# Kernel optimization log

Measured on AMD Instinct MI355X. Metric: run time of the kernel, lower is better.

The kernel has to match this reference:

```python
import jax, jax.numpy as jnp
import numpy as np

EMBED_DIM = 512
NUM_HEADS = 8
TGT_LEN = 1024
BSZ = 16


def setup_inputs() -> dict:
    key = jax.random.key(0)
    ks = jax.random.split(key, 6)
    E = EMBED_DIM
    query = jax.random.normal(ks[0], (TGT_LEN, BSZ, E), jnp.float32)
    i_proj = jax.random.normal(ks[1], (3 * E,), jnp.float32)
    # xavier_uniform-ish scale for (3E, E)
    lim = (6.0 / (3 * E + E)) ** 0.5
    in_proj_weight = jax.random.uniform(ks[2], (3 * E, E), jnp.float32, -lim, lim)
    in_proj_bias = jnp.zeros((3 * E,), jnp.float32)
    lim2 = (6.0 / (2 * E)) ** 0.5
    out_w = jax.random.uniform(ks[3], (E, E), jnp.float32, -lim2, lim2)
    out_b = jnp.zeros((E,), jnp.float32)
    bias_k = jax.random.normal(ks[4], (1, 1, E), jnp.float32)
    bias_v = jax.random.normal(ks[5], (1, 1, E), jnp.float32)
    return dict(query=query, i_proj=i_proj, in_proj_weight=in_proj_weight,
                in_proj_bias=in_proj_bias, out_w=out_w, out_b=out_b,
                bias_k=bias_k, bias_v=bias_v)


def reference(query, i_proj, in_proj_weight, in_proj_bias, out_w, out_b, bias_k, bias_v):
    # qkv_same path: key = value = query (self-attention)
    T, B, E = query.shape
    H = NUM_HEADS
    hd = E // H
    scaling = hd ** -0.5
    # per-call weight mutation: every 3rd column replaced by i_proj
    w = in_proj_weight.at[:, ::3].set(i_proj[:, None])
    qkv = jnp.einsum('tbe,fe->tbf', query, w) + in_proj_bias  # (T, B, 3E)
    q, k, v = jnp.split(qkv, 3, axis=-1)
    q = q * scaling
    k = jnp.concatenate([k, jnp.broadcast_to(bias_k, (1, B, E))], axis=0)  # (T+1, B, E)
    v = jnp.concatenate([v, jnp.broadcast_to(bias_v, (1, B, E))], axis=0)
    S = k.shape[0]
    q = q.reshape(T, B * H, hd).transpose(1, 0, 2)  # (B*H, T, hd)
    k = k.reshape(S, B * H, hd).transpose(1, 0, 2)  # (B*H, S, hd)
    v = v.reshape(S, B * H, hd).transpose(1, 0, 2)
    aw = jnp.einsum('nth,nsh->nts', q, k)  # (B*H, T, S)
    # global min-max normalization over the entire score tensor (not softmax)
    mn = jnp.min(aw)
    mx = jnp.max(aw)
    aw = (aw - mn) / (mx - mn)
    attn = jnp.einsum('nts,nsh->nth', aw, v)  # (B*H, T, hd)
    attn = attn.transpose(1, 0, 2).reshape(T, B, E)
    attn = attn @ out_w.T + out_b  # out_proj
    aw_avg = aw.reshape(B, H, T, S).sum(axis=1) / H  # (B, T, S)
    wq, wk, wv = jnp.split(w, 3, axis=0)
    w_ret = jnp.stack([wq.T, wk.T, wv.T], axis=0)  # (3, E, E)
    return attn, aw_avg, w_ret
```

## Files before the change

kernel.cpp:

```cpp
#include <hip/hip_runtime.h>
#include <hip/hip_bf16.h>
#include <stdint.h>

typedef __bf16 bf16;
typedef __bf16 bf16x8 __attribute__((ext_vector_type(8)));
typedef __bf16 bf16x4 __attribute__((ext_vector_type(4)));
typedef float  f32x4  __attribute__((ext_vector_type(4)));

#define MFMA_BF16(a,b,c) __builtin_amdgcn_mfma_f32_16x16x32_bf16((a),(b),(c),0,0,0)

#define WS_QBF_IN  0L
#define WS_WBF     16777216L
#define WS_OUTWBF  18350080L
#define WS_Q       18874368L
#define WS_K       35651584L
#define WS_V       52428800L
#define WS_VT      69206016L
#define WS_AWLAST  85983232L
#define WS_VCS     86507520L
#define WS_MM      86540288L
#define WS_KT      86540544L
#define WS_KTV     103317760L

__device__ __forceinline__ void gload16(const void* g, void* l) {
  __builtin_amdgcn_global_load_lds((const __attribute__((address_space(1))) uint32_t*)g,
                                   (__attribute__((address_space(3))) uint32_t*)l, 16, 0, 0);
}
__device__ __forceinline__ unsigned ordf(float x) {
  unsigned b = __float_as_uint(x);
  return (b & 0x80000000u) ? ~b : (b | 0x80000000u);
}
__device__ __forceinline__ float deordf(unsigned u) {
  unsigned b = (u & 0x80000000u) ? (u ^ 0x80000000u) : ~u;
  return __uint_as_float(b);
}

__global__ __launch_bounds__(256) void prep_all_kernel(
    const float* __restrict__ query, bf16* __restrict__ qbf_out,
    const float* __restrict__ in_w, const float* __restrict__ i_proj,
    const float* __restrict__ out_w, bf16* __restrict__ w_bf,
    bf16* __restrict__ outw_bf, float* __restrict__ w_ret,
    unsigned* __restrict__ mm) {
  long idx = (long)blockIdx.x * 256 + threadIdx.x;
  if (idx == 0) { mm[0] = 0xFFFFFFFFu; mm[1] = 0u; }
  if (idx < 786432L) {
    int f = (int)(idx >> 9), e = (int)(idx & 511);
    float val = (e % 3 == 0) ? i_proj[f] : in_w[idx];
    w_bf[idx] = (bf16)val;
    w_ret[(long)(f >> 9) * 262144 + (long)e * 512 + (f & 511)] = val;
  } else if (idx < 1048576L) {
    long j = idx - 786432L;
    outw_bf[j] = (bf16)out_w[j];
  }
#pragma unroll
  for (int it = 0; it < 2; ++it) {
    long i = idx + (long)it * 1048576L;
    float4 v = ((const float4*)query)[i];
    bf16x4 o; o[0] = (bf16)v.x; o[1] = (bf16)v.y; o[2] = (bf16)v.z; o[3] = (bf16)v.w;
    ((bf16x4*)qbf_out)[i] = o;
  }
}

#define PIPE_STAGE(Abase_, Bbase_, kk_, buf_)                                      \
  do {                                                                             \
    _Pragma("unroll")                                                              \
    for (int i_ = 0; i_ < 4; ++i_) {                                               \
      int c_ = tid + i_ * 256;                                                     \
      int row_ = c_ >> 3;                                                          \
      int cc_ = (c_ & 7) ^ (row_ & 7);                                             \
      gload16((Abase_) + (long)row_ * 512 + (kk_) + cc_ * 8,                       \
              (char*)aT[buf_] + (i_ * 256 + w * 64) * 16);                         \
      gload16((Bbase_) + (long)row_ * 512 + (kk_) + cc_ * 8,                       \
              (char*)bT[buf_] + (i_ * 256 + w * 64) * 16);                         \
    }                                                                              \
  } while (0)

#define PIPE_COMPUTE(buf_)                                                         \
  do {                                                                             \
    _Pragma("unroll")                                                              \
    for (int ks_ = 0; ks_ < 2; ++ks_) {                                            \
      bf16x8 af[4], bfr[4];                                                        \
      _Pragma("unroll")                                                            \
      for (int mi_ = 0; mi_ < 4; ++mi_) {                                          \
        int r_ = rm + mi_ * 16 + l15;                                              \
        int p_ = (ks_ * 4 + l4) ^ (r_ & 7);                                        \
        af[mi_] = *(const bf16x8*)((const char*)aT[buf_] + r_ * 128 + p_ * 16);    \
      }                                                                            \
      _Pragma("unroll")                                                            \
      for (int ni_ = 0; ni_ < 4; ++ni_) {                                          \
        int r_ = cn + ni_ * 16 + l15;                                              \
        int p_ = (ks_ * 4 + l4) ^ (r_ & 7);                                        \
        bfr[ni_] = *(const bf16x8*)((const char*)bT[buf_] + r_ * 128 + p_ * 16);   \
      }                                                                            \
      _Pragma("unroll")                                                            \
      for (int mi_ = 0; mi_ < 4; ++mi_)                                            \
        _Pragma("unroll")                                                          \
        for (int ni_ = 0; ni_ < 4; ++ni_)                                          \
          acc[mi_][ni_] = MFMA_BF16(af[mi_], bfr[ni_], acc[mi_][ni_]);             \
    }                                                                              \
  } while (0)

template <int MODE, int MINW>
__global__ __launch_bounds__(256, MINW) void gemm_kernel(
    const bf16* __restrict__ A, const bf16* __restrict__ B,
    const float* __restrict__ bias,
    bf16* __restrict__ q_out, bf16* __restrict__ k_out, bf16* __restrict__ v_out,
    float* __restrict__ outC) {
  __shared__ __align__(16) bf16 aT[2][128 * 64];
  __shared__ __align__(16) bf16 bT[2][128 * 64];
  const int tid = threadIdx.x;
  const int lane = tid & 63, w = tid >> 6;
  const int l15 = lane & 15, l4 = lane >> 4;
  const long r0 = (long)blockIdx.y * 128;
  const long f0 = (long)blockIdx.x * 128;
  const int rm = (w >> 1) * 64, cn = (w & 1) * 64;
  const bf16* Ab = A + r0 * 512;
  const bf16* Bb = B + f0 * 512;
  f32x4 acc[4][4] = {};

  PIPE_STAGE(Ab, Bb, 0, 0);
  PIPE_STAGE(Ab, Bb, 64, 1);
  asm volatile("s_waitcnt vmcnt(8)" ::: "memory");
  __builtin_amdgcn_s_barrier();
  __builtin_amdgcn_sched_barrier(0);
#pragma unroll
  for (int k = 0; k < 8; ++k) {
    PIPE_COMPUTE(k & 1);
    __builtin_amdgcn_s_barrier();
    __builtin_amdgcn_sched_barrier(0);
    if (k + 2 < 8) PIPE_STAGE(Ab, Bb, (k + 2) * 64, k & 1);
    if (k + 1 < 8) {
      if (k + 2 < 8) asm volatile("s_waitcnt vmcnt(8)" ::: "memory");
      else           asm volatile("s_waitcnt vmcnt(0)" ::: "memory");
      __builtin_amdgcn_s_barrier();
      __builtin_amdgcn_sched_barrier(0);
    }
  }
#pragma unroll
  for (int mi = 0; mi < 4; ++mi)
#pragma unroll
    for (int ni = 0; ni < 4; ++ni)
#pragma unroll
      for (int r = 0; r < 4; ++r) {
        long row = r0 + rm + mi * 16 + l4 * 4 + r;
        int f = (int)f0 + cn + ni * 16 + l15;
        float val = acc[mi][ni][r] + bias[f];
        if (MODE == 0) {
          int t = (int)(row >> 4), b = (int)(row & 15);
          int which = f >> 9, hh = (f >> 6) & 7, d = f & 63;
          long off = ((long)(b * 8 + hh) * 1024 + t) * 64 + d;
          if (which == 0)      q_out[off] = (bf16)(val * 0.125f);
          else if (which == 1) k_out[off] = (bf16)val;
          else                 v_out[off] = (bf16)val;
        } else {
          outC[row * 512 + f] = val;
        }
      }
}

__global__ __launch_bounds__(256, 2) void awsum_gemm_kernel(
    const bf16* __restrict__ q_bf, const bf16* __restrict__ k_bf,
    bf16* __restrict__ aw_raw, unsigned* __restrict__ mm) {
  __shared__ __align__(16) char wlds[4][16384];
  const int tid = threadIdx.x;
  const int lane = tid & 63, w = tid >> 6;
  const int l15 = lane & 15, l4 = lane >> 4;
  const int bid = blockIdx.x;
  const int xcd = bid & 7, slot = bid >> 3;
  const int b = xcd * 2 + (slot >> 6);
  const int rest = slot & 63;
  const int t0 = (rest >> 2) * 64;
  const int s0w = (rest & 3) * 256 + w * 64;
  char* lA = wlds[w];
  char* lB = wlds[w] + 8192;

  f32x4 acc[4][4] = {};
  f32x4 snap[4][4] = {};
  float vmin = 1e30f, vmax = -1e30f;

#define WAVE_STAGE(k_, buf_)                                                          \
  do {                                                                                \
    const int hh_ = (k_) >> 1, kh_ = ((k_) & 1) * 32;                                 \
    const bf16* qb_ = q_bf + ((long)(b * 8 + hh_) * 1024 + t0) * 64 + kh_;            \
    const bf16* kb_ = k_bf + ((long)(b * 8 + hh_) * 1024 + s0w) * 64 + kh_;           \
    _Pragma("unroll")                                                                 \
    for (int i_ = 0; i_ < 4; ++i_) {                                                  \
      int ci_ = lane + i_ * 64;                                                       \
      int row_ = ci_ >> 2, cc_ = ci_ & 3;                                             \
      int cc2_ = cc_ ^ ((row_ >> 1) & 3);                                             \
      gload16(qb_ + (long)row_ * 64 + cc2_ * 8, lA + (buf_) * 4096 + i_ * 1024);      \
      gload16(kb_ + (long)row_ * 64 + cc2_ * 8, lB + (buf_) * 4096 + i_ * 1024);      \
    }                                                                                 \
  } while (0)

#define WAVE_COMPUTE(buf_)                                                            \
  do {                                                                                \
    bf16x8 af[4], bfr[4];                                                             \
    _Pragma("unroll")                                                                 \
    for (int mi_ = 0; mi_ < 4; ++mi_) {                                               \
      int r_ = mi_ * 16 + l15;                                                        \
      int p_ = l4 ^ ((r_ >> 1) & 3);                                                  \
      af[mi_] = *(const bf16x8*)(lA + (buf_) * 4096 + r_ * 64 + p_ * 16);             \
    }                                                                                 \
    _Pragma("unroll")                                                                 \
    for (int ni_ = 0; ni_ < 4; ++ni_) {                                               \
      int r_ = ni_ * 16 + l15;                                                        \
      int p_ = l4 ^ ((r_ >> 1) & 3);                                                  \
      bfr[ni_] = *(const bf16x8*)(lB + (buf_) * 4096 + r_ * 64 + p_ * 16);            \
    }                                                                                 \
    _Pragma("unroll")                                                                 \
    for (int mi_ = 0; mi_ < 4; ++mi_)                                                 \
      _Pragma("unroll")                                                               \
      for (int ni_ = 0; ni_ < 4; ++ni_)                                               \
        acc[mi_][ni_] = MFMA_BF16(af[mi_], bfr[ni_], acc[mi_][ni_]);                  \
  } while (0)

  WAVE_STAGE(0, 0);
  WAVE_STAGE(1, 1);
#pragma unroll
  for (int k = 0; k < 16; ++k) {
    if (k < 15) asm volatile("s_waitcnt vmcnt(8)" ::: "memory");
    else        asm volatile("s_waitcnt vmcnt(0)" ::: "memory");
    __builtin_amdgcn_sched_barrier(0);
    WAVE_COMPUTE(k & 1);
    if (k & 1) {
#pragma unroll
      for (int mi = 0; mi < 4; ++mi)
#pragma unroll
        for (int ni = 0; ni < 4; ++ni) {
          f32x4 d = acc[mi][ni] - snap[mi][ni];
#pragma unroll
          for (int r = 0; r < 4; ++r) {
            vmin = fminf(vmin, d[r]);
            vmax = fmaxf(vmax, d[r]);
          }
          snap[mi][ni] = acc[mi][ni];
        }
    }
    if (k + 2 < 16) {
      asm volatile("s_waitcnt lgkmcnt(0)" ::: "memory");
      __builtin_amdgcn_sched_barrier(0);
      WAVE_STAGE(k + 2, k & 1);
    }
  }
#pragma unroll
  for (int mi = 0; mi < 4; ++mi)
#pragma unroll
    for (int ni = 0; ni < 4; ++ni)
#pragma unroll
      for (int r = 0; r < 4; ++r) {
        int t = t0 + mi * 16 + l4 * 4 + r;
        int s = s0w + ni * 16 + l15;
        aw_raw[((long)b * 1024 + t) * 1024 + s] = (bf16)acc[mi][ni][r];
      }
#pragma unroll
  for (int off = 32; off; off >>= 1) {
    vmin = fminf(vmin, __shfl_xor(vmin, off));
    vmax = fmaxf(vmax, __shfl_xor(vmax, off));
  }
  if (lane == 0) { atomicMin(&mm[0], ordf(vmin)); atomicMax(&mm[1], ordf(vmax)); }
#undef WAVE_STAGE
#undef WAVE_COMPUTE
}

__global__ __launch_bounds__(256) void transpose_kv_kernel(
    const bf16* __restrict__ k_bf, const bf16* __restrict__ v_bf,
    bf16* __restrict__ kT, bf16* __restrict__ vT) {
  const bf16* src = blockIdx.z ? v_bf : k_bf;
  bf16* dst = blockIdx.z ? vT : kT;
  const int n = blockIdx.y;
  const long s0 = (long)blockIdx.x * 64;
  __shared__ __align__(16) bf16 tile[64][72];
  const int tid = threadIdx.x;
  const int row = tid >> 3, cc = tid & 7;
#pragma unroll
  for (int it = 0; it < 2; ++it) {
    int r = row + it * 32;
    bf16x8 vv = *(const bf16x8*)(src + ((long)n * 1024 + s0 + r) * 64 + cc * 8);
    *(bf16x8*)&tile[r][cc * 8] = vv;
  }
  __syncthreads();
#pragma unroll
  for (int it = 0; it < 2; ++it) {
    int d = row + it * 32;
    bf16x8 ov;
#pragma unroll
    for (int j = 0; j < 8; ++j) ov[j] = tile[cc * 8 + j][d];
    *(bf16x8*)(dst + ((long)n * 64 + d) * 1024 + s0 + cc * 8) = ov;
  }
}

__global__ __launch_bounds__(256) void reduce_small_kernel(
    const bf16* __restrict__ vT, const float* __restrict__ bias_v,
    float* __restrict__ vcs, const bf16* __restrict__ q_bf,
    const float* __restrict__ bias_k, float* __restrict__ aw_last,
    unsigned* __restrict__ mm) {
  if (blockIdx.x < 128) {
    const int n = blockIdx.x, h = n & 7;
    const int d = threadIdx.x >> 2, q = threadIdx.x & 3;
    float acc = 0.f;
    const bf16* row = vT + (long)n * 65536 + (long)d * 1024 + q * 256;
#pragma unroll 4
    for (int j = 0; j < 32; ++j) {
      bf16x8 v = *(const bf16x8*)(row + j * 8);
#pragma unroll
      for (int e = 0; e < 8; ++e) acc += (float)v[e];
    }
    __shared__ float red[256];
    red[threadIdx.x] = acc;
    __syncthreads();
    if (q == 0)
      vcs[n * 64 + d] = red[d * 4] + red[d * 4 + 1] + red[d * 4 + 2] + red[d * 4 + 3] +
                        bias_v[h * 64 + d];
  } else {
    const int lin = blockIdx.x - 128;
    const int bx = lin & 3, n = lin >> 2, h = n & 7;
    const int t = bx * 256 + threadIdx.x;
    float acc = 0.f;
    const bf16* qrow = q_bf + ((long)n * 1024 + t) * 64;
#pragma unroll
    for (int j = 0; j < 8; ++j) {
      bf16x8 qv = *(const bf16x8*)(qrow + j * 8);
#pragma unroll
      for (int e = 0; e < 8; ++e) acc += (float)qv[e] * bias_k[h * 64 + j * 8 + e];
    }
    aw_last[(long)n * 1024 + t] = acc;
    float vmin = acc, vmax = acc;
#pragma unroll
    for (int off = 32; off; off >>= 1) {
      vmin = fminf(vmin, __shfl_xor(vmin, off));
      vmax = fmaxf(vmax, __shfl_xor(vmax, off));
    }
    if ((threadIdx.x & 63) == 0) { atomicMin(&mm[0], ordf(vmin)); atomicMax(&mm[1], ordf(vmax)); }
  }
}

__global__ __launch_bounds__(256) void ktv_kernel(const bf16* __restrict__ kT,
                                                  const bf16* __restrict__ vT,
                                                  bf16* __restrict__ ktvT) {
  const int n = blockIdx.x;
  const int tid = threadIdx.x;
  const int lane = tid & 63, w = tid >> 6;
  const int l15 = lane & 15, l4 = lane >> 4;
  const int wr = w >> 1, wc = w & 1;
  f32x4 acc[2][2] = {};
  const bf16* kbase = kT + (long)n * 65536;
  const bf16* vbase = vT + (long)n * 65536;
  for (int s0 = 0; s0 < 1024; s0 += 32) {
    bf16x8 af[2], bfr[2];
#pragma unroll
    for (int mi = 0; mi < 2; ++mi)
      af[mi] = *(const bf16x8*)(kbase + (long)(wr * 32 + mi * 16 + l15) * 1024 + s0 + l4 * 8);
#pragma unroll
    for (int ni = 0; ni < 2; ++ni)
      bfr[ni] = *(const bf16x8*)(vbase + (long)(wc * 32 + ni * 16 + l15) * 1024 + s0 + l4 * 8);
#pragma unroll
    for (int mi = 0; mi < 2; ++mi)
#pragma unroll
      for (int ni = 0; ni < 2; ++ni)
        acc[mi][ni] = MFMA_BF16(af[mi], bfr[ni], acc[mi][ni]);
  }
#pragma unroll
  for (int mi = 0; mi < 2; ++mi)
#pragma unroll
    for (int ni = 0; ni < 2; ++ni)
#pragma unroll
      for (int r = 0; r < 4; ++r) {
        int d = wr * 32 + mi * 16 + l4 * 4 + r;
        int dp = wc * 32 + ni * 16 + l15;
        ktvT[(long)n * 4096 + dp * 64 + d] = (bf16)acc[mi][ni][r];
      }
}

__global__ __launch_bounds__(256) void qattn_kernel(
    const bf16* __restrict__ q_bf, const bf16* __restrict__ ktvT,
    const float* __restrict__ aw_last, const float* __restrict__ vcs,
    const float* __restrict__ bias_v, const unsigned* __restrict__ mm,
    bf16* __restrict__ A2) {
  const int tid = threadIdx.x;
  const int lane = tid & 63, w = tid >> 6;
  const int l15 = lane & 15, l4 = lane >> 4;
  const int t0 = blockIdx.x * 64;
  const int h = blockIdx.y * 4 + w;
  const int b = blockIdx.z;
  const long n = (long)b * 8 + h;
  f32x4 acc[4][4] = {};
  const bf16* qbase = q_bf + (n * 1024 + t0) * 64;
  const bf16* kbase = ktvT + (long)n * 4096;
#pragma unroll
  for (int kk = 0; kk < 64; kk += 32) {
    bf16x8 af[4], bfr[4];
#pragma unroll
    for (int mi = 0; mi < 4; ++mi)
      af[mi] = *(const bf16x8*)(qbase + (mi * 16 + l15) * 64 + kk + l4 * 8);
#pragma unroll
    for (int ni = 0; ni < 4; ++ni)
      bfr[ni] = *(const bf16x8*)(kbase + (ni * 16 + l15) * 64 + kk + l4 * 8);
#pragma unroll
    for (int mi = 0; mi < 4; ++mi)
#pragma unroll
      for (int ni = 0; ni < 4; ++ni)
        acc[mi][ni] = MFMA_BF16(af[mi], bfr[ni], acc[mi][ni]);
  }
  float mn = deordf(mm[0]), mx = deordf(mm[1]);
  float a = 1.f / (mx - mn), c = -mn * a;
#pragma unroll
  for (int mi = 0; mi < 4; ++mi)
#pragma unroll
    for (int r = 0; r < 4; ++r) {
      int t = t0 + mi * 16 + l4 * 4 + r;
      float alast = a * aw_last[n * 1024 + t];
#pragma unroll
      for (int ni = 0; ni < 4; ++ni) {
        int dp = ni * 16 + l15;
        float val = a * acc[mi][ni][r] + alast * bias_v[h * 64 + dp] + c * vcs[n * 64 + dp];
        A2[((long)t * 16 + b) * 512 + h * 64 + dp] = (bf16)val;
      }
    }
}

__global__ __launch_bounds__(256) void rescale_kernel(const bf16* __restrict__ aw_raw,
                                                      float* __restrict__ aw_out,
                                                      const float* __restrict__ aw_last,
                                                      const unsigned* __restrict__ mm) {
  long idx = (long)blockIdx.x * 256 + threadIdx.x;
  float mn = deordf(mm[0]), mx = deordf(mm[1]);
  float a = 1.f / (mx - mn), c = -mn * a;
  int s = (int)(idx % 1025);
  long bt = idx / 1025;
  float v;
  if (s < 1024) {
    v = (float)aw_raw[bt * 1024 + s];
  } else {
    int b = (int)(bt >> 10), t = (int)(bt & 1023);
    v = 0.f;
#pragma unroll
    for (int h = 0; h < 8; ++h) v += aw_last[(long)(b * 8 + h) * 1024 + t];
  }
  aw_out[idx] = fmaf(a, v * 0.125f, c);
}

extern "C" void kernel_launch(void* const* d_in, const int* in_sizes, int n_in,
                              void* d_out, int out_size, void* d_ws, size_t ws_size,
                              hipStream_t stream) {
  const float* query  = (const float*)d_in[0];
  const float* i_proj = (const float*)d_in[1];
  const float* in_w   = (const float*)d_in[2];
  const float* in_b   = (const float*)d_in[3];
  const float* out_w  = (const float*)d_in[4];
  const float* out_b  = (const float*)d_in[5];
  const float* bias_k = (const float*)d_in[6];
  const float* bias_v = (const float*)d_in[7];
  float* out = (float*)d_out;

  char* ws = (char*)d_ws;
  bf16* qbf_in = (bf16*)(ws + WS_QBF_IN);
  bf16* w_bf   = (bf16*)(ws + WS_WBF);
  bf16* outwbf = (bf16*)(ws + WS_OUTWBF);
  bf16* q_bf   = (bf16*)(ws + WS_Q);
  bf16* k_bf   = (bf16*)(ws + WS_K);
  bf16* v_bf   = (bf16*)(ws + WS_V);
  bf16* vT     = (bf16*)(ws + WS_VT);
  bf16* kT     = (bf16*)(ws + WS_KT);
  bf16* ktvT   = (bf16*)(ws + WS_KTV);
  bf16* aw_raw = (bf16*)(ws + WS_V);
  float* aw_last = (float*)(ws + WS_AWLAST);
  float* vcs     = (float*)(ws + WS_VCS);
  unsigned* mm   = (unsigned*)(ws + WS_MM);
  bf16* A2 = qbf_in;

  float* out_attn  = out;
  float* out_awavg = out + 8388608L;
  float* out_wret  = out + 25182208L;

  prep_all_kernel<<<4096, 256, 0, stream>>>(query, qbf_in, in_w, i_proj, out_w,
                                            w_bf, outwbf, out_wret, mm);
  gemm_kernel<0, 3><<<dim3(12, 128), 256, 0, stream>>>(qbf_in, w_bf, in_b,
                                                       q_bf, k_bf, v_bf, nullptr);
  transpose_kv_kernel<<<dim3(16, 128, 2), 256, 0, stream>>>(k_bf, v_bf, kT, vT);
  reduce_small_kernel<<<640, 256, 0, stream>>>(vT, bias_v, vcs, q_bf, bias_k, aw_last, mm);
  ktv_kernel<<<128, 256, 0, stream>>>(kT, vT, ktvT);
  awsum_gemm_kernel<<<1024, 256, 0, stream>>>(q_bf, k_bf, aw_raw, mm);
  rescale_kernel<<<65600, 256, 0, stream>>>(aw_raw, out_awavg, aw_last, mm);
  qattn_kernel<<<dim3(16, 2, 16), 256, 0, stream>>>(q_bf, ktvT, aw_last, vcs, bias_v, mm, A2);
  gemm_kernel<1, 2><<<dim3(4, 128), 256, 0, stream>>>(A2, outwbf, out_b,
                                                      nullptr, nullptr, nullptr, out_attn);
}
```

Before: 300.7 us.

## Load Q fragments straight to registers and pack head-sum in bf16 for occupancy

The per-head score GEMM kernel no longer stages Q through LDS: each wave loads its A fragments directly from global memory into double-buffered registers, which halves per-wave LDS. The fp32 snapshot array used to recover per-head scores is replaced by a running head-sum kept as packed bf16 pairs, with the accumulator reset after each head. Launch bounds go from 2 to 3 blocks per CU. The intent is higher occupancy from fewer registers and less LDS. The trade-offs are uncoalesced direct global loads for Q and rounding the running head-sum to bf16 after every head, which adds accumulation error.

```diff
diff --git a/kernel.cpp b/kernel.cpp
--- a/kernel.cpp
+++ b/kernel.cpp
@@ -5,6 +5,7 @@
 typedef __bf16 bf16;
 typedef __bf16 bf16x8 __attribute__((ext_vector_type(8)));
 typedef __bf16 bf16x4 __attribute__((ext_vector_type(4)));
+typedef __bf16 bf16x2 __attribute__((ext_vector_type(2)));
 typedef float  f32x4  __attribute__((ext_vector_type(4)));
 
 #define MFMA_BF16(a,b,c) __builtin_amdgcn_mfma_f32_16x16x32_bf16((a),(b),(c),0,0,0)
@@ -158,10 +159,10 @@
       }
 }
 
-__global__ __launch_bounds__(256, 2) void awsum_gemm_kernel(
+__global__ __launch_bounds__(256, 3) void awsum_gemm_kernel(
     const bf16* __restrict__ q_bf, const bf16* __restrict__ k_bf,
     bf16* __restrict__ aw_raw, unsigned* __restrict__ mm) {
-  __shared__ __align__(16) char wlds[4][16384];
+  __shared__ __align__(16) char wlds[4][8192];
   const int tid = threadIdx.x;
   const int lane = tid & 63, w = tid >> 6;
   const int l15 = lane & 15, l4 = lane >> 4;
@@ -171,37 +172,37 @@
   const int rest = slot & 63;
   const int t0 = (rest >> 2) * 64;
   const int s0w = (rest & 3) * 256 + w * 64;
-  char* lA = wlds[w];
-  char* lB = wlds[w] + 8192;
+  char* lB = wlds[w];
 
   f32x4 acc[4][4] = {};
-  f32x4 snap[4][4] = {};
+  unsigned hs[32] = {};
   float vmin = 1e30f, vmax = -1e30f;
 
-#define WAVE_STAGE(k_, buf_)                                                          \
+#define BSTAGE(k_, buf_)                                                              \
   do {                                                                                \
     const int hh_ = (k_) >> 1, kh_ = ((k_) & 1) * 32;                                 \
-    const bf16* qb_ = q_bf + ((long)(b * 8 + hh_) * 1024 + t0) * 64 + kh_;            \
     const bf16* kb_ = k_bf + ((long)(b * 8 + hh_) * 1024 + s0w) * 64 + kh_;           \
     _Pragma("unroll")                                                                 \
     for (int i_ = 0; i_ < 4; ++i_) {                                                  \
       int ci_ = lane + i_ * 64;                                                       \
       int row_ = ci_ >> 2, cc_ = ci_ & 3;                                             \
       int cc2_ = cc_ ^ ((row_ >> 1) & 3);                                             \
-      gload16(qb_ + (long)row_ * 64 + cc2_ * 8, lA + (buf_) * 4096 + i_ * 1024);      \
       gload16(kb_ + (long)row_ * 64 + cc2_ * 8, lB + (buf_) * 4096 + i_ * 1024);      \
     }                                                                                 \
   } while (0)
 
-#define WAVE_COMPUTE(buf_)                                                            \
+#define ALOAD(k_, af_)                                                                \
   do {                                                                                \
-    bf16x8 af[4], bfr[4];                                                             \
+    const int hh_ = (k_) >> 1, kh_ = ((k_) & 1) * 32;                                 \
+    const bf16* qb_ = q_bf + ((long)(b * 8 + hh_) * 1024 + t0) * 64 + kh_;            \
     _Pragma("unroll")                                                                 \
-    for (int mi_ = 0; mi_ < 4; ++mi_) {                                               \
-      int r_ = mi_ * 16 + l15;                                                        \
-      int p_ = l4 ^ ((r_ >> 1) & 3);                                                  \
-      af[mi_] = *(const bf16x8*)(lA + (buf_) * 4096 + r_ * 64 + p_ * 16);             \
-    }                                                                                 \
+    for (int mi_ = 0; mi_ < 4; ++mi_)                                                 \
+      af_[mi_] = *(const bf16x8*)(qb_ + (long)(mi_ * 16 + l15) * 64 + l4 * 8);        \
+  } while (0)
+
+#define WCOMPUTE(buf_, af_)                                                           \
+  do {                                                                                \
+    bf16x8 bfr[4];                                                                    \
     _Pragma("unroll")                                                                 \
     for (int ni_ = 0; ni_ < 4; ++ni_) {                                               \
       int r_ = ni_ * 16 + l15;                                                        \
@@ -212,35 +213,45 @@
     for (int mi_ = 0; mi_ < 4; ++mi_)                                                 \
       _Pragma("unroll")                                                               \
       for (int ni_ = 0; ni_ < 4; ++ni_)                                               \
-        acc[mi_][ni_] = MFMA_BF16(af[mi_], bfr[ni_], acc[mi_][ni_]);                  \
+        acc[mi_][ni_] = MFMA_BF16(af_[mi_], bfr[ni_], acc[mi_][ni_]);                 \
   } while (0)
 
-  WAVE_STAGE(0, 0);
-  WAVE_STAGE(1, 1);
+  bf16x8 afA[4], afB[4];
+  BSTAGE(0, 0);
+  BSTAGE(1, 1);
+  ALOAD(0, afA);
 #pragma unroll
   for (int k = 0; k < 16; ++k) {
-    if (k < 15) asm volatile("s_waitcnt vmcnt(8)" ::: "memory");
-    else        asm volatile("s_waitcnt vmcnt(0)" ::: "memory");
+    if (k + 1 < 16) { if (k & 1) ALOAD(k + 1, afA); else ALOAD(k + 1, afB); }
+    if (k == 0)      asm volatile("s_waitcnt vmcnt(4)" ::: "memory");
+    else if (k < 15) asm volatile("s_waitcnt vmcnt(8)" ::: "memory");
+    else             asm volatile("s_waitcnt vmcnt(0)" ::: "memory");
     __builtin_amdgcn_sched_barrier(0);
-    WAVE_COMPUTE(k & 1);
+    if (k & 1) WCOMPUTE(k & 1, afB); else WCOMPUTE(k & 1, afA);
     if (k & 1) {
 #pragma unroll
       for (int mi = 0; mi < 4; ++mi)
 #pragma unroll
         for (int ni = 0; ni < 4; ++ni) {
-          f32x4 d = acc[mi][ni] - snap[mi][ni];
-#pragma unroll
-          for (int r = 0; r < 4; ++r) {
-            vmin = fminf(vmin, d[r]);
-            vmax = fmaxf(vmax, d[r]);
+#pragma unroll
+          for (int r = 0; r < 4; r += 2) {
+            float v0 = acc[mi][ni][r], v1 = acc[mi][ni][r + 1];
+            vmin = fminf(vmin, fminf(v0, v1));
+            vmax = fmaxf(vmax, fmaxf(v0, v1));
+            int hi = (mi * 4 + ni) * 2 + (r >> 1);
+            float o0 = __uint_as_float(hs[hi] << 16) + v0;
+            float o1 = __uint_as_float(hs[hi] & 0xFFFF0000u) + v1;
+            bf16x2 pk; pk[0] = (bf16)o0; pk[1] = (bf16)o1;
+            unsigned u; __builtin_memcpy(&u, &pk, 4);
+            hs[hi] = u;
           }
-          snap[mi][ni] = acc[mi][ni];
+          acc[mi][ni] = (f32x4){0.f, 0.f, 0.f, 0.f};
         }
     }
     if (k + 2 < 16) {
       asm volatile("s_waitcnt lgkmcnt(0)" ::: "memory");
       __builtin_amdgcn_sched_barrier(0);
-      WAVE_STAGE(k + 2, k & 1);
+      BSTAGE(k + 2, k & 1);
     }
   }
 #pragma unroll
@@ -249,9 +260,12 @@
     for (int ni = 0; ni < 4; ++ni)
 #pragma unroll
       for (int r = 0; r < 4; ++r) {
+        unsigned h = hs[(mi * 4 + ni) * 2 + (r >> 1)];
+        unsigned short us = (unsigned short)((r & 1) ? (h >> 16) : (h & 0xFFFFu));
+        bf16 val; __builtin_memcpy(&val, &us, 2);
         int t = t0 + mi * 16 + l4 * 4 + r;
         int s = s0w + ni * 16 + l15;
-        aw_raw[((long)b * 1024 + t) * 1024 + s] = (bf16)acc[mi][ni][r];
+        aw_raw[((long)b * 1024 + t) * 1024 + s] = val;
       }
 #pragma unroll
   for (int off = 32; off; off >>= 1) {
@@ -259,8 +273,9 @@
     vmax = fmaxf(vmax, __shfl_xor(vmax, off));
   }
   if (lane == 0) { atomicMin(&mm[0], ordf(vmin)); atomicMax(&mm[1], ordf(vmax)); }
-#undef WAVE_STAGE
-#undef WAVE_COMPUTE
+#undef BSTAGE
+#undef ALOAD
+#undef WCOMPUTE
 }
 
 __global__ __launch_bounds__(256) void transpose_kv_kernel(
```

Result: slower. 372.4 us (+23.8%).
